# Optimization experiments

Hardware: AMD Instinct MI355X
Metric: run time of the kernel (lower is better)

Reference implementation:

```python
import jax, jax.numpy as jnp
import numpy as np

N = 40000
IN_DIM = 128
HID = 64
E = 640000


def sage_conv(x, edge_index, W_l, b_l, W_r):
    """PyG SAGEConv with mean aggregation.
    out = lin_l(mean_{j in N(i)} x_j) + lin_r(x_i)
    edge_index[0]=src (message source), edge_index[1]=dst (aggregation target).
    """
    src, dst = edge_index[0], edge_index[1]
    n = x.shape[0]
    msgs = x[src]                                            # [E, d] gather
    sums = jax.ops.segment_sum(msgs, dst, num_segments=n)    # [N, d]
    cnt = jax.ops.segment_sum(jnp.ones((msgs.shape[0],), x.dtype), dst,
                              num_segments=n)                # [N]
    mean = sums / jnp.maximum(cnt, 1.0)[:, None]
    return mean @ W_l.T + b_l + x @ W_r.T


def setup_inputs() -> dict:
    key = jax.random.key(0)
    ks = jax.random.split(key, 8)
    x = jax.random.normal(ks[0], (N, IN_DIM), dtype=jnp.float32)
    edge_index = jax.random.randint(ks[1], (2, E), 0, N, dtype=jnp.int32)
    s1 = 1.0 / np.sqrt(IN_DIM)
    s2 = 1.0 / np.sqrt(HID)
    W1_l = jax.random.uniform(ks[2], (HID, IN_DIM), jnp.float32, -s1, s1)
    b1_l = jax.random.uniform(ks[3], (HID,), jnp.float32, -s1, s1)
    W1_r = jax.random.uniform(ks[4], (HID, IN_DIM), jnp.float32, -s1, s1)
    W2_l = jax.random.uniform(ks[5], (HID, HID), jnp.float32, -s2, s2)
    b2_l = jax.random.uniform(ks[6], (HID,), jnp.float32, -s2, s2)
    W2_r = jax.random.uniform(ks[7], (HID, HID), jnp.float32, -s2, s2)
    return {"x": x, "edge_index": edge_index,
            "W1_l": W1_l, "b1_l": b1_l, "W1_r": W1_r,
            "W2_l": W2_l, "b2_l": b2_l, "W2_r": W2_r}


def reference(x, edge_index, W1_l, b1_l, W1_r, W2_l, b2_l, W2_r):
    h = sage_conv(x, edge_index, W1_l, b1_l, W1_r)
    h = jax.nn.relu(h)
    # dropout is identity in eval mode (reference baseline is deterministic)
    z = sage_conv(h, edge_index, W2_l, b2_l, W2_r)
    return z
```

## Files before the change

kernel.cpp:

```cpp
#include <hip/hip_runtime.h>

#define INDIM 128
#define HID 64
#define CAP 64
#define GEMM_BLOCKS 625
#define BIN_BLOCKS 256
#define PREP_BLOCKS 32
#define RSH 7
#define RMASK ((1 << RSH) - 1)
#define NRANGE 313
#define SBCAP 28

__device__ __forceinline__ unsigned short f2bf(float f) {
    union { float f; unsigned int i; } c; c.f = f;
    return (unsigned short)((c.i + 0x7FFFu + ((c.i >> 16) & 1u)) >> 16);
}

__device__ __forceinline__ void aggF(const unsigned short* __restrict__ T,
                                     int idxv, int deg, int f2,
                                     float& a0, float& a1) {
    const int eo = (threadIdx.x & 63) >> 5;
    for (int s = 0; s < deg; s += 8) {
        #pragma unroll
        for (int u = 0; u < 4; ++u) {
            const int e = s + u * 2 + eo;
            int sidx = __shfl(idxv, e, 64);
            const bool live = (e < deg);
            sidx = live ? sidx : 0;
            const unsigned uu = *(const unsigned*)&T[(size_t)sidx * 64 + f2 * 2];
            union { unsigned i; float f; } clo, chi;
            clo.i = uu << 16;
            chi.i = uu & 0xffff0000u;
            a0 += live ? clo.f : 0.f;
            a1 += live ? chi.f : 0.f;
        }
    }
    a0 += __shfl_xor(a0, 32, 64);
    a1 += __shfl_xor(a1, 32, 64);
}


__global__ __launch_bounds__(256) void k_bin_prep(
    const int* __restrict__ src, const int* __restrict__ dst,
    unsigned int* __restrict__ hist_global, unsigned int* __restrict__ ebin,
    const float* __restrict__ W1l, const float* __restrict__ W1r,
    const float* __restrict__ W2l, const float* __restrict__ W2r,
    float* __restrict__ WT1l, float* __restrict__ WT1r,
    float* __restrict__ WT2l, float* __restrict__ WT2r, int E) {
    const int tid = threadIdx.x;

    if (blockIdx.x >= BIN_BLOCKS) {
        const int gtid = (blockIdx.x - BIN_BLOCKS) * 256 + tid;
        if (gtid < 64 * 128) {
            int j = gtid >> 7, k = gtid & 127;
            WT1l[k * 64 + j] = W1l[gtid];
            WT1r[k * 64 + j] = W1r[gtid];
        }
        if (gtid < 64 * 64) {
            int j = gtid >> 6, k = gtid & 63;
            WT2l[k * 64 + j] = W2l[gtid];
            WT2r[k * 64 + j] = W2r[gtid];
        }
        return;
    }

    __shared__ unsigned int hist[NRANGE];
    __shared__ unsigned int cur[NRANGE];
    const int b = blockIdx.x;
    const int ech = (E + BIN_BLOCKS - 1) / BIN_BLOCKS;
    const int e0 = b * ech;
    const int e1 = (e0 + ech < E) ? e0 + ech : E;

    for (int r = tid; r < NRANGE; r += 256) { hist[r] = 0; cur[r] = 0; }
    __syncthreads();
    for (int e = e0 + tid; e < e1; e += 256)
        atomicAdd(&hist[((unsigned)dst[e]) >> RSH], 1u);
    __syncthreads();
    for (int r = tid; r < NRANGE; r += 256)
        hist_global[(size_t)r * BIN_BLOCKS + b] = hist[r];
    __syncthreads();
    for (int e = e0 + tid; e < e1; e += 256) {
        const unsigned d = (unsigned)dst[e];
        const unsigned s = (unsigned)src[e];
        const unsigned r = d >> RSH;
        const unsigned off = atomicAdd(&cur[r], 1u);
        if (off < SBCAP)
            ebin[((size_t)r * BIN_BLOCKS + b) * SBCAP + off] = (d << 16) | s;
    }
}


__global__ __launch_bounds__(256) void k_gemm1_place(
    const float* __restrict__ A,
    const float* __restrict__ WTl, const float* __restrict__ WTr,
    unsigned short* __restrict__ Pb, float* __restrict__ Q,
    const unsigned int* __restrict__ hist_global,
    const unsigned int* __restrict__ ebin,
    int* __restrict__ cnt, unsigned short* __restrict__ sorted, int N) {
    __shared__ float As[64][INDIM + 1];
    __shared__ unsigned int lcnt[1 << RSH];
    const int tid = threadIdx.x;

    if (blockIdx.x < NRANGE) {
        const int r = blockIdx.x;
        if (tid < (1 << RSH)) lcnt[tid] = 0;
        __syncthreads();
        const int lane = tid & 63, w = tid >> 6;
        const int sb_local = lane >> 3, ent0 = lane & 7;
        for (int g = w * 8; g < BIN_BLOCKS; g += 32) {
            const int sb = g + sb_local;
            unsigned c = hist_global[(size_t)r * BIN_BLOCKS + sb];
            if (c > SBCAP) c = SBCAP;
            const unsigned int* eb = ebin + ((size_t)r * BIN_BLOCKS + sb) * SBCAP;
            for (unsigned p = 0; p * 8 < c; ++p) {
                const unsigned e = p * 8 + ent0;
                if (e < c) {
                    const unsigned pkt = eb[e];
                    const unsigned d = pkt >> 16;
                    const unsigned slot = atomicAdd(&lcnt[d & RMASK], 1u);
                    if (slot < CAP)
                        sorted[(d << 6) + slot] = (unsigned short)(pkt & 0xffffu);
                }
            }
        }
        __syncthreads();
        for (int l = tid; l < (1 << RSH); l += 256) {
            const int node = (r << RSH) + l;
            if (node < N) cnt[node] = (int)lcnt[l];
        }
        return;
    }

    const int bm = (blockIdx.x - NRANGE) * 64;
    for (int idx = tid; idx < 64 * 32; idx += 256) {
        int row = idx >> 5, kq = idx & 31;
        const float4 v = ((const float4*)A)[(size_t)(bm + row) * 32 + kq];
        As[row][kq * 4 + 0] = v.x; As[row][kq * 4 + 1] = v.y;
        As[row][kq * 4 + 2] = v.z; As[row][kq * 4 + 3] = v.w;
    }
    __syncthreads();

    const int tx = tid & 15, ty = tid >> 4;
    const int n0 = ty * 4;
    float accl[4][4] = {}, accr[4][4] = {};
    #pragma unroll 8
    for (int k = 0; k < INDIM; ++k) {
        float a[4];
        #pragma unroll
        for (int i = 0; i < 4; ++i) a[i] = As[n0 + i][k];
        const float4 blv = ((const float4*)WTl)[k * 16 + tx];
        const float4 brv = ((const float4*)WTr)[k * 16 + tx];
        const float bl[4] = {blv.x, blv.y, blv.z, blv.w};
        const float br[4] = {brv.x, brv.y, brv.z, brv.w};
        #pragma unroll
        for (int i = 0; i < 4; ++i) {
            #pragma unroll
            for (int j = 0; j < 4; ++j) {
                accl[i][j] += a[i] * bl[j];
                accr[i][j] += a[i] * br[j];
            }
        }
    }
    #pragma unroll
    for (int i = 0; i < 4; ++i) {
        int m = bm + n0 + i;
        ushort4 pv;
        pv.x = f2bf(accl[i][0]); pv.y = f2bf(accl[i][1]);
        pv.z = f2bf(accl[i][2]); pv.w = f2bf(accl[i][3]);
        ((ushort4*)Pb)[(size_t)m * 16 + tx] = pv;
        ((float4*)Q)[(size_t)m * 16 + tx] =
            make_float4(accr[i][0], accr[i][1], accr[i][2], accr[i][3]);
    }
}


__global__ __launch_bounds__(256) void k_agg1(
    const unsigned short* __restrict__ Pb, const float* __restrict__ Q,
    const float* __restrict__ b1,
    const int* __restrict__ cnt, const unsigned short* __restrict__ sorted,
    unsigned short* __restrict__ Hb, float* __restrict__ H, int N) {
    const int wid  = (blockIdx.x * 256 + threadIdx.x) >> 6;
    const int lane = threadIdx.x & 63;
    const int f2 = lane & 31;
    if (wid >= N) return;
    int deg = cnt[wid]; if (deg > CAP) deg = CAP;
    const int idxv = (int)sorted[(wid << 6) + lane];
    float a0 = 0.f, a1 = 0.f;
    aggF(Pb, idxv, deg, f2, a0, a1);
    if (lane < 32) {
        const float inv = 1.0f / fmaxf((float)deg, 1.0f);
        const float2 qv = *(const float2*)&Q[(size_t)wid * 64 + f2 * 2];
        const float2 bv = *(const float2*)&b1[f2 * 2];
        const float h0 = fmaxf(a0 * inv + bv.x + qv.x, 0.f);
        const float h1 = fmaxf(a1 * inv + bv.y + qv.y, 0.f);
        *(unsigned*)&Hb[(size_t)wid * 64 + f2 * 2] =
            (unsigned)f2bf(h0) | ((unsigned)f2bf(h1) << 16);
        *(float2*)&H[(size_t)wid * 64 + f2 * 2] = make_float2(h0, h1);
    }
}


__global__ __launch_bounds__(256) void k_agg2h(
    const unsigned short* __restrict__ Hb,
    const int* __restrict__ cnt, const unsigned short* __restrict__ sorted,
    float* __restrict__ meanH, int N) {
    const int wid  = (blockIdx.x * 256 + threadIdx.x) >> 6;
    const int lane = threadIdx.x & 63;
    const int f2 = lane & 31;
    if (wid >= N) return;
    int deg = cnt[wid]; if (deg > CAP) deg = CAP;
    const int idxv = (int)sorted[(wid << 6) + lane];
    float a0 = 0.f, a1 = 0.f;
    aggF(Hb, idxv, deg, f2, a0, a1);
    if (lane < 32) {
        const float inv = 1.0f / fmaxf((float)deg, 1.0f);
        *(float2*)&meanH[(size_t)wid * 64 + f2 * 2] =
            make_float2(a0 * inv, a1 * inv);
    }
}


__global__ __launch_bounds__(256) void k_gemm_z(
    const float* __restrict__ meanH, const float* __restrict__ H,
    const float* __restrict__ WTl, const float* __restrict__ WTr,
    const float* __restrict__ b2, float* __restrict__ z, int N) {
    __shared__ float As1[64][HID + 1];
    __shared__ float As2[64][HID + 1];
    const int tid = threadIdx.x;
    const int bm = blockIdx.x * 64;
    for (int idx = tid; idx < 64 * 16; idx += 256) {
        int row = idx >> 4, kq = idx & 15;
        const float4 v1 = ((const float4*)meanH)[(size_t)(bm + row) * 16 + kq];
        const float4 v2 = ((const float4*)H)[(size_t)(bm + row) * 16 + kq];
        As1[row][kq * 4 + 0] = v1.x; As1[row][kq * 4 + 1] = v1.y;
        As1[row][kq * 4 + 2] = v1.z; As1[row][kq * 4 + 3] = v1.w;
        As2[row][kq * 4 + 0] = v2.x; As2[row][kq * 4 + 1] = v2.y;
        As2[row][kq * 4 + 2] = v2.z; As2[row][kq * 4 + 3] = v2.w;
    }
    __syncthreads();

    const int tx = tid & 15, ty = tid >> 4;
    const int n0 = ty * 4;
    float acc[4][4] = {};
    #pragma unroll 8
    for (int k = 0; k < HID; ++k) {
        float a1[4], a2[4];
        #pragma unroll
        for (int i = 0; i < 4; ++i) { a1[i] = As1[n0 + i][k]; a2[i] = As2[n0 + i][k]; }
        const float4 blv = ((const float4*)WTl)[k * 16 + tx];
        const float4 brv = ((const float4*)WTr)[k * 16 + tx];
        const float bl[4] = {blv.x, blv.y, blv.z, blv.w};
        const float br[4] = {brv.x, brv.y, brv.z, brv.w};
        #pragma unroll
        for (int i = 0; i < 4; ++i) {
            #pragma unroll
            for (int j = 0; j < 4; ++j)
                acc[i][j] += a1[i] * bl[j] + a2[i] * br[j];
        }
    }
    const float4 bv = *(const float4*)&b2[tx * 4];
    #pragma unroll
    for (int i = 0; i < 4; ++i) {
        int m = bm + n0 + i;
        if (m < N) {
            ((float4*)z)[(size_t)m * 16 + tx] =
                make_float4(acc[i][0] + bv.x, acc[i][1] + bv.y,
                            acc[i][2] + bv.z, acc[i][3] + bv.w);
        }
    }
}


extern "C" void kernel_launch(void* const* d_in, const int* in_sizes, int n_in,
                              void* d_out, int out_size, void* d_ws, size_t ws_size,
                              hipStream_t stream) {
    const float* x   = (const float*)d_in[0];
    const int*  edge = (const int*)d_in[1];
    const float* W1l = (const float*)d_in[2];
    const float* b1l = (const float*)d_in[3];
    const float* W1r = (const float*)d_in[4];
    const float* W2l = (const float*)d_in[5];
    const float* b2l = (const float*)d_in[6];
    const float* W2r = (const float*)d_in[7];

    const int N = in_sizes[0] / INDIM;
    const int E = in_sizes[1] / 2;
    const int* src = edge;
    const int* dst = edge + E;

    char* w = (char*)d_ws;
    auto carve = [&](size_t bytes) {
        char* p = w; w += (bytes + 255) & ~(size_t)255; return p;
    };
    unsigned short* Pb  = (unsigned short*)carve((size_t)N * 64 * 2);
    unsigned short* Hb  = (unsigned short*)carve((size_t)N * 64 * 2);
    float* Q     = (float*)carve((size_t)N * 64 * 4);
    float* H     = (float*)carve((size_t)N * 64 * 4);
    float* meanH = (float*)carve((size_t)N * 64 * 4);
    float* WT1l = (float*)carve(128 * 64 * 4);
    float* WT1r = (float*)carve(128 * 64 * 4);
    float* WT2l = (float*)carve(64 * 64 * 4);
    float* WT2r = (float*)carve(64 * 64 * 4);
    int* cnt    = (int*)carve((size_t)N * 4);
    unsigned short* sorted = (unsigned short*)carve((size_t)N * CAP * 2);
    unsigned int* hist_global = (unsigned int*)carve((size_t)NRANGE * BIN_BLOCKS * 4);
    unsigned int* ebin = (unsigned int*)carve((size_t)NRANGE * BIN_BLOCKS * SBCAP * 4);

    float* zout = (float*)d_out;

    const int gT = (N + 63) / 64;
    const int gW = (N * 64 + 255) / 256;

    k_bin_prep<<<BIN_BLOCKS + PREP_BLOCKS, 256, 0, stream>>>(
        src, dst, hist_global, ebin,
        W1l, W1r, W2l, W2r, WT1l, WT1r, WT2l, WT2r, E);
    k_gemm1_place<<<NRANGE + GEMM_BLOCKS, 256, 0, stream>>>(
        x, WT1l, WT1r, Pb, Q, hist_global, ebin, cnt, sorted, N);
    k_agg1<<<gW, 256, 0, stream>>>(Pb, Q, b1l, cnt, sorted, Hb, H, N);
    k_agg2h<<<gW, 256, 0, stream>>>(Hb, cnt, sorted, meanH, N);
    k_gemm_z<<<gT, 256, 0, stream>>>(meanH, H, WT2l, WT2r, b2l, zout, N);
}
```

Measured before the change: 108.8 us.

## Fuse layer-1 agg, layer-2 agg and final GEMM into one persistent kernel with grid barriers

Replaces three separate launches (agg1, agg2h, gemm_z) with one persistent kernel of 1024 blocks. Each block strides over nodes for the two aggregation phases and over 32-row tiles for the final GEMM, with a software grid barrier (atomic counter plus spin) between phases. The barrier counter is reset in the prep kernel. This removes two kernel launch gaps and tail effects, at the cost of relying on all 1024 blocks being co-resident, spin-wait overhead, and smaller GEMM tiles.

```diff
diff --git a/kernel.cpp b/kernel.cpp
--- a/kernel.cpp
+++ b/kernel.cpp
@@ -10,6 +10,8 @@
 #define RMASK ((1 << RSH) - 1)
 #define NRANGE 313
 #define SBCAP 28
+#define TGRID 1024
+#define TWAVES (TGRID * 4)
 
 __device__ __forceinline__ unsigned short f2bf(float f) {
     union { float f; unsigned int i; } c; c.f = f;
@@ -39,6 +41,18 @@
     a1 += __shfl_xor(a1, 32, 64);
 }
 
+__device__ __forceinline__ void gbar(unsigned int* bar, unsigned target) {
+    __syncthreads();
+    if (threadIdx.x == 0) {
+        __threadfence();
+        atomicAdd(bar, 1u);
+        while (__hip_atomic_load(bar, __ATOMIC_ACQUIRE,
+                                 __HIP_MEMORY_SCOPE_AGENT) < target)
+            __builtin_amdgcn_s_sleep(8);
+    }
+    __syncthreads();
+}
+
 
 __global__ __launch_bounds__(256) void k_bin_prep(
     const int* __restrict__ src, const int* __restrict__ dst,
@@ -46,11 +60,13 @@
     const float* __restrict__ W1l, const float* __restrict__ W1r,
     const float* __restrict__ W2l, const float* __restrict__ W2r,
     float* __restrict__ WT1l, float* __restrict__ WT1r,
-    float* __restrict__ WT2l, float* __restrict__ WT2r, int E) {
+    float* __restrict__ WT2l, float* __restrict__ WT2r,
+    unsigned int* __restrict__ bar, int E) {
     const int tid = threadIdx.x;
 
     if (blockIdx.x >= BIN_BLOCKS) {
         const int gtid = (blockIdx.x - BIN_BLOCKS) * 256 + tid;
+        if (gtid == 0) *bar = 0;
         if (gtid < 64 * 128) {
             int j = gtid >> 7, k = gtid & 127;
             WT1l[k * 64 + j] = W1l[gtid];
@@ -174,99 +190,99 @@
 }
 
 
-__global__ __launch_bounds__(256) void k_agg1(
+__global__ __launch_bounds__(256, 8) void k_tail(
     const unsigned short* __restrict__ Pb, const float* __restrict__ Q,
     const float* __restrict__ b1,
     const int* __restrict__ cnt, const unsigned short* __restrict__ sorted,
-    unsigned short* __restrict__ Hb, float* __restrict__ H, int N) {
-    const int wid  = (blockIdx.x * 256 + threadIdx.x) >> 6;
-    const int lane = threadIdx.x & 63;
+    unsigned short* __restrict__ Hb, float* __restrict__ H,
+    float* __restrict__ meanH,
+    const float* __restrict__ WTl, const float* __restrict__ WTr,
+    const float* __restrict__ b2, float* __restrict__ z,
+    unsigned int* __restrict__ bar, int N) {
+    __shared__ float As1[32][HID + 1];
+    __shared__ float As2[32][HID + 1];
+    const int tid = threadIdx.x;
+    const int lane = tid & 63;
     const int f2 = lane & 31;
-    if (wid >= N) return;
-    int deg = cnt[wid]; if (deg > CAP) deg = CAP;
-    const int idxv = (int)sorted[(wid << 6) + lane];
-    float a0 = 0.f, a1 = 0.f;
-    aggF(Pb, idxv, deg, f2, a0, a1);
-    if (lane < 32) {
-        const float inv = 1.0f / fmaxf((float)deg, 1.0f);
-        const float2 qv = *(const float2*)&Q[(size_t)wid * 64 + f2 * 2];
-        const float2 bv = *(const float2*)&b1[f2 * 2];
-        const float h0 = fmaxf(a0 * inv + bv.x + qv.x, 0.f);
-        const float h1 = fmaxf(a1 * inv + bv.y + qv.y, 0.f);
-        *(unsigned*)&Hb[(size_t)wid * 64 + f2 * 2] =
-            (unsigned)f2bf(h0) | ((unsigned)f2bf(h1) << 16);
-        *(float2*)&H[(size_t)wid * 64 + f2 * 2] = make_float2(h0, h1);
-    }
-}
-
-
-__global__ __launch_bounds__(256) void k_agg2h(
-    const unsigned short* __restrict__ Hb,
-    const int* __restrict__ cnt, const unsigned short* __restrict__ sorted,
-    float* __restrict__ meanH, int N) {
-    const int wid  = (blockIdx.x * 256 + threadIdx.x) >> 6;
-    const int lane = threadIdx.x & 63;
-    const int f2 = lane & 31;
-    if (wid >= N) return;
-    int deg = cnt[wid]; if (deg > CAP) deg = CAP;
-    const int idxv = (int)sorted[(wid << 6) + lane];
-    float a0 = 0.f, a1 = 0.f;
-    aggF(Hb, idxv, deg, f2, a0, a1);
-    if (lane < 32) {
-        const float inv = 1.0f / fmaxf((float)deg, 1.0f);
-        *(float2*)&meanH[(size_t)wid * 64 + f2 * 2] =
-            make_float2(a0 * inv, a1 * inv);
-    }
-}
-
-
-__global__ __launch_bounds__(256) void k_gemm_z(
-    const float* __restrict__ meanH, const float* __restrict__ H,
-    const float* __restrict__ WTl, const float* __restrict__ WTr,
-    const float* __restrict__ b2, float* __restrict__ z, int N) {
-    __shared__ float As1[64][HID + 1];
-    __shared__ float As2[64][HID + 1];
-    const int tid = threadIdx.x;
-    const int bm = blockIdx.x * 64;
-    for (int idx = tid; idx < 64 * 16; idx += 256) {
-        int row = idx >> 4, kq = idx & 15;
-        const float4 v1 = ((const float4*)meanH)[(size_t)(bm + row) * 16 + kq];
-        const float4 v2 = ((const float4*)H)[(size_t)(bm + row) * 16 + kq];
-        As1[row][kq * 4 + 0] = v1.x; As1[row][kq * 4 + 1] = v1.y;
-        As1[row][kq * 4 + 2] = v1.z; As1[row][kq * 4 + 3] = v1.w;
-        As2[row][kq * 4 + 0] = v2.x; As2[row][kq * 4 + 1] = v2.y;
-        As2[row][kq * 4 + 2] = v2.z; As2[row][kq * 4 + 3] = v2.w;
-    }
-    __syncthreads();
-
+    const int gw = blockIdx.x * 4 + (tid >> 6);
+
+    for (int wid = gw; wid < N; wid += TWAVES) {
+        int deg = cnt[wid]; if (deg > CAP) deg = CAP;
+        const int idxv = (int)sorted[(wid << 6) + lane];
+        float a0 = 0.f, a1 = 0.f;
+        aggF(Pb, idxv, deg, f2, a0, a1);
+        if (lane < 32) {
+            const float inv = 1.0f / fmaxf((float)deg, 1.0f);
+            const float2 qv = *(const float2*)&Q[(size_t)wid * 64 + f2 * 2];
+            const float2 bv = *(const float2*)&b1[f2 * 2];
+            const float h0 = fmaxf(a0 * inv + bv.x + qv.x, 0.f);
+            const float h1 = fmaxf(a1 * inv + bv.y + qv.y, 0.f);
+            *(unsigned*)&Hb[(size_t)wid * 64 + f2 * 2] =
+                (unsigned)f2bf(h0) | ((unsigned)f2bf(h1) << 16);
+            *(float2*)&H[(size_t)wid * 64 + f2 * 2] = make_float2(h0, h1);
+        }
+    }
+    gbar(bar, TGRID);
+
+    for (int wid = gw; wid < N; wid += TWAVES) {
+        int deg = cnt[wid]; if (deg > CAP) deg = CAP;
+        const int idxv = (int)sorted[(wid << 6) + lane];
+        float a0 = 0.f, a1 = 0.f;
+        aggF(Hb, idxv, deg, f2, a0, a1);
+        if (lane < 32) {
+            const float inv = 1.0f / fmaxf((float)deg, 1.0f);
+            *(float2*)&meanH[(size_t)wid * 64 + f2 * 2] =
+                make_float2(a0 * inv, a1 * inv);
+        }
+    }
+    gbar(bar, 2 * TGRID);
+
+    const int ntile = (N + 31) >> 5;
     const int tx = tid & 15, ty = tid >> 4;
-    const int n0 = ty * 4;
-    float acc[4][4] = {};
-    #pragma unroll 8
-    for (int k = 0; k < HID; ++k) {
-        float a1[4], a2[4];
+    for (int t = blockIdx.x; t < ntile; t += TGRID) {
+        const int bm = t * 32;
+        for (int idx = tid; idx < 32 * 16; idx += 256) {
+            int row = idx >> 4, kq = idx & 15;
+            const float4 v1 = ((const float4*)meanH)[(size_t)(bm + row) * 16 + kq];
+            const float4 v2 = ((const float4*)H)[(size_t)(bm + row) * 16 + kq];
+            As1[row][kq * 4 + 0] = v1.x; As1[row][kq * 4 + 1] = v1.y;
+            As1[row][kq * 4 + 2] = v1.z; As1[row][kq * 4 + 3] = v1.w;
+            As2[row][kq * 4 + 0] = v2.x; As2[row][kq * 4 + 1] = v2.y;
+            As2[row][kq * 4 + 2] = v2.z; As2[row][kq * 4 + 3] = v2.w;
+        }
+        __syncthreads();
+
+        const int n0 = ty * 2;
+        float acc[2][4] = {};
+        #pragma unroll 8
+        for (int k = 0; k < HID; ++k) {
+            float a1v[2], a2v[2];
+            #pragma unroll
+            for (int i = 0; i < 2; ++i) {
+                a1v[i] = As1[n0 + i][k]; a2v[i] = As2[n0 + i][k];
+            }
+            const float4 blv = ((const float4*)WTl)[k * 16 + tx];
+            const float4 brv = ((const float4*)WTr)[k * 16 + tx];
+            const float bl[4] = {blv.x, blv.y, blv.z, blv.w};
+            const float br[4] = {brv.x, brv.y, brv.z, brv.w};
+            #pragma unroll
+            for (int i = 0; i < 2; ++i) {
+                #pragma unroll
+                for (int j = 0; j < 4; ++j)
+                    acc[i][j] += a1v[i] * bl[j] + a2v[i] * br[j];
+            }
+        }
+        const float4 bv = *(const float4*)&b2[tx * 4];
         #pragma unroll
-        for (int i = 0; i < 4; ++i) { a1[i] = As1[n0 + i][k]; a2[i] = As2[n0 + i][k]; }
-        const float4 blv = ((const float4*)WTl)[k * 16 + tx];
-        const float4 brv = ((const float4*)WTr)[k * 16 + tx];
-        const float bl[4] = {blv.x, blv.y, blv.z, blv.w};
-        const float br[4] = {brv.x, brv.y, brv.z, brv.w};
-        #pragma unroll
-        for (int i = 0; i < 4; ++i) {
-            #pragma unroll
-            for (int j = 0; j < 4; ++j)
-                acc[i][j] += a1[i] * bl[j] + a2[i] * br[j];
-        }
-    }
-    const float4 bv = *(const float4*)&b2[tx * 4];
-    #pragma unroll
-    for (int i = 0; i < 4; ++i) {
-        int m = bm + n0 + i;
-        if (m < N) {
-            ((float4*)z)[(size_t)m * 16 + tx] =
-                make_float4(acc[i][0] + bv.x, acc[i][1] + bv.y,
-                            acc[i][2] + bv.z, acc[i][3] + bv.w);
-        }
+        for (int i = 0; i < 2; ++i) {
+            const int m = bm + n0 + i;
+            if (m < N) {
+                ((float4*)z)[(size_t)m * 16 + tx] =
+                    make_float4(acc[i][0] + bv.x, acc[i][1] + bv.y,
+                                acc[i][2] + bv.z, acc[i][3] + bv.w);
+            }
+        }
+        __syncthreads();
     }
 }
 
@@ -305,18 +321,16 @@
     unsigned short* sorted = (unsigned short*)carve((size_t)N * CAP * 2);
     unsigned int* hist_global = (unsigned int*)carve((size_t)NRANGE * BIN_BLOCKS * 4);
     unsigned int* ebin = (unsigned int*)carve((size_t)NRANGE * BIN_BLOCKS * SBCAP * 4);
+    unsigned int* bar  = (unsigned int*)carve(256);
 
     float* zout = (float*)d_out;
-
-    const int gT = (N + 63) / 64;
-    const int gW = (N * 64 + 255) / 256;
 
     k_bin_prep<<<BIN_BLOCKS + PREP_BLOCKS, 256, 0, stream>>>(
         src, dst, hist_global, ebin,
-        W1l, W1r, W2l, W2r, WT1l, WT1r, WT2l, WT2r, E);
+        W1l, W1r, W2l, W2r, WT1l, WT1r, WT2l, WT2r, bar, E);
     k_gemm1_place<<<NRANGE + GEMM_BLOCKS, 256, 0, stream>>>(
         x, WT1l, WT1r, Pb, Q, hist_global, ebin, cnt, sorted, N);
-    k_agg1<<<gW, 256, 0, stream>>>(Pb, Q, b1l, cnt, sorted, Hb, H, N);
-    k_agg2h<<<gW, 256, 0, stream>>>(Hb, cnt, sorted, meanH, N);
-    k_gemm_z<<<gT, 256, 0, stream>>>(meanH, H, WT2l, WT2r, b2l, zout, N);
-}
+    k_tail<<<TGRID, 256, 0, stream>>>(
+        Pb, Q, b1l, cnt, sorted, Hb, H, meanH,
+        WT2l, WT2r, b2l, zout, bar, N);
+}
```

New measurement: 380.6 us. 3.5x slower.

## Aggregate two nodes per wavefront with 8-byte bf16 gathers

Applied to the files above, without the earlier changes.

The two aggregation kernels now give each 64-lane wavefront two destination nodes instead of one. Lanes split into four groups of 16, and each lane reads four bf16 features (8 bytes) per neighbor, so 4 neighbors are fetched per step for each node. A two-stage cross-lane shuffle reduction combines the partial sums. This raises memory-level parallelism and halves the wave count, at the cost of more registers, extra shuffles, and divergence when the two nodes have different degrees.

```diff
diff --git a/kernel.cpp b/kernel.cpp
--- a/kernel.cpp
+++ b/kernel.cpp
@@ -11,32 +11,51 @@
 #define NRANGE 313
 #define SBCAP 28
 
+__device__ __forceinline__ float bf2f(unsigned short u) {
+    union { unsigned int i; float f; } c; c.i = ((unsigned int)u) << 16; return c.f;
+}
 __device__ __forceinline__ unsigned short f2bf(float f) {
     union { float f; unsigned int i; } c; c.f = f;
     return (unsigned short)((c.i + 0x7FFFu + ((c.i >> 16) & 1u)) >> 16);
 }
 
-__device__ __forceinline__ void aggF(const unsigned short* __restrict__ T,
-                                     int idxv, int deg, int f2,
-                                     float& a0, float& a1) {
-    const int eo = (threadIdx.x & 63) >> 5;
-    for (int s = 0; s < deg; s += 8) {
+__device__ __forceinline__ void agg2n(const unsigned short* __restrict__ T,
+                                      int idxA, int idxB, int degA, int degB,
+                                      int q, int f4,
+                                      float aA[4], float aB[4]) {
+    const int ncA = (degA + 3) >> 2, ncB = (degB + 3) >> 2;
+    const int ncM = ncA > ncB ? ncA : ncB;
+    for (int c = 0; c < ncM; c += 4) {
         #pragma unroll
         for (int u = 0; u < 4; ++u) {
-            const int e = s + u * 2 + eo;
-            int sidx = __shfl(idxv, e, 64);
-            const bool live = (e < deg);
-            sidx = live ? sidx : 0;
-            const unsigned uu = *(const unsigned*)&T[(size_t)sidx * 64 + f2 * 2];
-            union { unsigned i; float f; } clo, chi;
-            clo.i = uu << 16;
-            chi.i = uu & 0xffff0000u;
-            a0 += live ? clo.f : 0.f;
-            a1 += live ? chi.f : 0.f;
-        }
-    }
-    a0 += __shfl_xor(a0, 32, 64);
-    a1 += __shfl_xor(a1, 32, 64);
+            const int lanesel = (c + u) * 4 + q;
+            int sA = __shfl(idxA, lanesel, 64);
+            int sB = __shfl(idxB, lanesel, 64);
+            const bool lA = lanesel < degA;
+            const bool lB = lanesel < degB;
+            sA = lA ? sA : 0;
+            sB = lB ? sB : 0;
+            const uint2 vA = *(const uint2*)&T[(size_t)sA * 64 + f4 * 4];
+            const uint2 vB = *(const uint2*)&T[(size_t)sB * 64 + f4 * 4];
+            const float mA = lA ? 1.f : 0.f;
+            const float mB = lB ? 1.f : 0.f;
+            aA[0] += bf2f((unsigned short)(vA.x & 0xffffu)) * mA;
+            aA[1] += bf2f((unsigned short)(vA.x >> 16)) * mA;
+            aA[2] += bf2f((unsigned short)(vA.y & 0xffffu)) * mA;
+            aA[3] += bf2f((unsigned short)(vA.y >> 16)) * mA;
+            aB[0] += bf2f((unsigned short)(vB.x & 0xffffu)) * mB;
+            aB[1] += bf2f((unsigned short)(vB.x >> 16)) * mB;
+            aB[2] += bf2f((unsigned short)(vB.y & 0xffffu)) * mB;
+            aB[3] += bf2f((unsigned short)(vB.y >> 16)) * mB;
+        }
+    }
+    #pragma unroll
+    for (int j = 0; j < 4; ++j) {
+        aA[j] += __shfl_xor(aA[j], 16, 64);
+        aA[j] += __shfl_xor(aA[j], 32, 64);
+        aB[j] += __shfl_xor(aB[j], 16, 64);
+        aB[j] += __shfl_xor(aB[j], 32, 64);
+    }
 }
 
 
@@ -179,23 +198,35 @@
     const float* __restrict__ b1,
     const int* __restrict__ cnt, const unsigned short* __restrict__ sorted,
     unsigned short* __restrict__ Hb, float* __restrict__ H, int N) {
-    const int wid  = (blockIdx.x * 256 + threadIdx.x) >> 6;
+    const int wave = (blockIdx.x * 256 + threadIdx.x) >> 6;
     const int lane = threadIdx.x & 63;
-    const int f2 = lane & 31;
-    if (wid >= N) return;
-    int deg = cnt[wid]; if (deg > CAP) deg = CAP;
-    const int idxv = (int)sorted[(wid << 6) + lane];
-    float a0 = 0.f, a1 = 0.f;
-    aggF(Pb, idxv, deg, f2, a0, a1);
-    if (lane < 32) {
+    const int q = lane >> 4, f4 = lane & 15;
+    const int nA = wave * 2, nB = nA + 1;
+    if (nA >= N) return;
+    int dv = (lane < 2 && nA + lane < N) ? cnt[nA + lane] : 0;
+    int degA = __shfl(dv, 0, 64); degA = degA > CAP ? CAP : degA;
+    int degB = __shfl(dv, 1, 64); degB = degB > CAP ? CAP : degB;
+    const int idxA = (int)sorted[(nA << 6) + lane];
+    const int idxB = (nB < N) ? (int)sorted[(nB << 6) + lane] : 0;
+    float aA[4] = {}, aB[4] = {};
+    agg2n(Pb, idxA, idxB, degA, degB, q, f4, aA, aB);
+
+    const int node = (q == 0) ? nA : nB;
+    const float* ap = (q == 0) ? aA : aB;
+    const int deg = (q == 0) ? degA : degB;
+    if ((q == 0 || q == 1) && node < N) {
         const float inv = 1.0f / fmaxf((float)deg, 1.0f);
-        const float2 qv = *(const float2*)&Q[(size_t)wid * 64 + f2 * 2];
-        const float2 bv = *(const float2*)&b1[f2 * 2];
-        const float h0 = fmaxf(a0 * inv + bv.x + qv.x, 0.f);
-        const float h1 = fmaxf(a1 * inv + bv.y + qv.y, 0.f);
-        *(unsigned*)&Hb[(size_t)wid * 64 + f2 * 2] =
-            (unsigned)f2bf(h0) | ((unsigned)f2bf(h1) << 16);
-        *(float2*)&H[(size_t)wid * 64 + f2 * 2] = make_float2(h0, h1);
+        const float4 qv = *(const float4*)&Q[(size_t)node * 64 + f4 * 4];
+        const float4 bv = *(const float4*)&b1[f4 * 4];
+        const float h0 = fmaxf(ap[0] * inv + bv.x + qv.x, 0.f);
+        const float h1 = fmaxf(ap[1] * inv + bv.y + qv.y, 0.f);
+        const float h2 = fmaxf(ap[2] * inv + bv.z + qv.z, 0.f);
+        const float h3 = fmaxf(ap[3] * inv + bv.w + qv.w, 0.f);
+        uint2 u;
+        u.x = (unsigned)f2bf(h0) | ((unsigned)f2bf(h1) << 16);
+        u.y = (unsigned)f2bf(h2) | ((unsigned)f2bf(h3) << 16);
+        *(uint2*)&Hb[(size_t)node * 64 + f4 * 4] = u;
+        *(float4*)&H[(size_t)node * 64 + f4 * 4] = make_float4(h0, h1, h2, h3);
     }
 }
 
@@ -204,18 +235,26 @@
     const unsigned short* __restrict__ Hb,
     const int* __restrict__ cnt, const unsigned short* __restrict__ sorted,
     float* __restrict__ meanH, int N) {
-    const int wid  = (blockIdx.x * 256 + threadIdx.x) >> 6;
+    const int wave = (blockIdx.x * 256 + threadIdx.x) >> 6;
     const int lane = threadIdx.x & 63;
-    const int f2 = lane & 31;
-    if (wid >= N) return;
-    int deg = cnt[wid]; if (deg > CAP) deg = CAP;
-    const int idxv = (int)sorted[(wid << 6) + lane];
-    float a0 = 0.f, a1 = 0.f;
-    aggF(Hb, idxv, deg, f2, a0, a1);
-    if (lane < 32) {
+    const int q = lane >> 4, f4 = lane & 15;
+    const int nA = wave * 2, nB = nA + 1;
+    if (nA >= N) return;
+    int dv = (lane < 2 && nA + lane < N) ? cnt[nA + lane] : 0;
+    int degA = __shfl(dv, 0, 64); degA = degA > CAP ? CAP : degA;
+    int degB = __shfl(dv, 1, 64); degB = degB > CAP ? CAP : degB;
+    const int idxA = (int)sorted[(nA << 6) + lane];
+    const int idxB = (nB < N) ? (int)sorted[(nB << 6) + lane] : 0;
+    float aA[4] = {}, aB[4] = {};
+    agg2n(Hb, idxA, idxB, degA, degB, q, f4, aA, aB);
+
+    const int node = (q == 0) ? nA : nB;
+    const float* ap = (q == 0) ? aA : aB;
+    const int deg = (q == 0) ? degA : degB;
+    if ((q == 0 || q == 1) && node < N) {
         const float inv = 1.0f / fmaxf((float)deg, 1.0f);
-        *(float2*)&meanH[(size_t)wid * 64 + f2 * 2] =
-            make_float2(a0 * inv, a1 * inv);
+        *(float4*)&meanH[(size_t)node * 64 + f4 * 4] =
+            make_float4(ap[0] * inv, ap[1] * inv, ap[2] * inv, ap[3] * inv);
     }
 }
 
@@ -309,14 +348,15 @@
     float* zout = (float*)d_out;
 
     const int gT = (N + 63) / 64;
-    const int gW = (N * 64 + 255) / 256;
+    const int nwave = (N + 1) / 2;
+    const int gW2 = (nwave + 3) / 4;
 
     k_bin_prep<<<BIN_BLOCKS + PREP_BLOCKS, 256, 0, stream>>>(
         src, dst, hist_global, ebin,
         W1l, W1r, W2l, W2r, WT1l, WT1r, WT2l, WT2r, E);
     k_gemm1_place<<<NRANGE + GEMM_BLOCKS, 256, 0, stream>>>(
         x, WT1l, WT1r, Pb, Q, hist_global, ebin, cnt, sorted, N);
-    k_agg1<<<gW, 256, 0, stream>>>(Pb, Q, b1l, cnt, sorted, Hb, H, N);
-    k_agg2h<<<gW, 256, 0, stream>>>(Hb, cnt, sorted, meanH, N);
+    k_agg1<<<gW2, 256, 0, stream>>>(Pb, Q, b1l, cnt, sorted, Hb, H, N);
+    k_agg2h<<<gW2, 256, 0, stream>>>(Hb, cnt, sorted, meanH, N);
     k_gemm_z<<<gT, 256, 0, stream>>>(meanH, H, WT2l, WT2r, b2l, zout, N);
 }
```

Result: faster. 102.9 us (median of 2 runs) (-5.4%).
